# Performance work log

Measured on AMD Instinct MI355X. Metric: run time of the kernel, lower is better.

## Reference

```python
import math
import jax, jax.numpy as jnp
import numpy as np

D_MODEL = 1024
D_STATE = 32
DT_MIN = 0.001
DT_MAX = 0.1
SEQ_LEN = 4096


def setup_inputs() -> dict:
    key = jax.random.key(0)
    kB, kC, kdt = jax.random.split(key, 3)
    log_A_real = jnp.full((D_MODEL, D_STATE), math.log(0.5), dtype=jnp.float32)
    A_imag = jnp.broadcast_to(jnp.linspace(0.0, math.pi, D_STATE, dtype=jnp.float32)[None, :],
                              (D_MODEL, D_STATE)).copy()
    B = jax.random.normal(kB, (D_MODEL, D_STATE, 2), dtype=jnp.float32)
    C = jax.random.normal(kC, (D_MODEL, D_STATE, 2), dtype=jnp.float32)
    log_dt = (jax.random.uniform(kdt, (D_MODEL,), dtype=jnp.float32)
              * (math.log(DT_MAX) - math.log(DT_MIN)) + math.log(DT_MIN))
    return {"log_A_real": log_A_real, "A_imag": A_imag, "B": B, "C": C,
            "log_dt": log_dt, "L": SEQ_LEN}


def reference(log_A_real, A_imag, B, C, log_dt, L):
    # ZOH-discretized diagonal SSM kernel: K[d,l] = Re(sum_n C[d,n] B[d,n] A_bar[d,n]^l)
    dt = jax.nn.softplus(log_dt)                      # (d,)
    A_real = -jax.nn.softplus(log_A_real)             # (d,n) forced negative
    A = jax.lax.complex(A_real, A_imag)               # (d,n) complex64
    A_bar = jnp.exp(dt[:, None] * A)                  # (d,n)
    Bc = jax.lax.complex(B[..., 0], B[..., 1])        # (d,n)
    Cc = jax.lax.complex(C[..., 0], C[..., 1])        # (d,n)
    l = jnp.arange(L, dtype=jnp.float32)              # (L,)
    # A_bar^l via exp(l*log(A_bar)); log(A_bar)=dt*A exactly since |dt*A_imag|<pi
    A_pow = jnp.exp((dt[:, None] * A)[:, :, None] * l)  # (d,n,L) Vandermonde
    K = jnp.einsum('dn,dnl->dl', Cc * Bc, A_pow).real   # (d,L)
    return K
```

## Files before the change

kernel.cpp:

```cpp
#include <hip/hip_runtime.h>
#include <math.h>

#define N_STATE 32

typedef _Float16 f16;
typedef f16 f16x8 __attribute__((ext_vector_type(8)));
typedef float f32x4 __attribute__((ext_vector_type(4)));

__device__ __forceinline__ unsigned swz(int row, int byte_in_row) {
  return (unsigned)(((row << 7) + byte_in_row) ^ ((row & 7) << 4));
}

__device__ __forceinline__ unsigned oswz(unsigned word) {
  return word ^ (((word >> 6) & 7u) << 2);
}

__device__ __forceinline__ float softplus_hw(float x) {
  const float t = __builtin_amdgcn_exp2f(x * 1.4426950408889634f);
  return 0.6931471805599453f * __builtin_amdgcn_logf(1.0f + t);
}

__global__ __launch_bounds__(256) void s4d_mfma_kernel(
    const float* __restrict__ log_A_real,
    const float* __restrict__ A_imag,
    const float* __restrict__ Bp,
    const float* __restrict__ Cp,
    const float* __restrict__ log_dt,
    float* __restrict__ K,
    int L) {
  const int d = blockIdx.x;
  const int tid = threadIdx.x;

  __shared__ float s_wrl2e[N_STATE], s_wirev[N_STATE];
  __shared__ float s_gr[N_STATE], s_gi[N_STATE];
  __shared__ __align__(16) char s_tab[2][64 * 128];
  f16* s_U = (f16*)s_tab[0];
  f16* s_V = (f16*)s_tab[1];
  float* s_out = (float*)s_tab;

  if (tid < N_STATE) {
    const int n = tid;
    const int idx = d * N_STATE + n;
    const float dt = softplus_hw(log_dt[d]);
    const float wr = -dt * softplus_hw(log_A_real[idx]);
    const float wi = dt * A_imag[idx];
    s_wrl2e[n] = wr * 1.4426950408889634f;
    s_wirev[n] = wi * 0.15915494309189535f;
    const float br = Bp[2 * idx], bi = Bp[2 * idx + 1];
    const float cr = Cp[2 * idx], ci = Cp[2 * idx + 1];
    s_gr[n] = cr * br - ci * bi;
    s_gi[n] = cr * bi + ci * br;
  }
  __syncthreads();

  {
    const int uh = tid >> 7;
    const int idx = tid & 127;
    const int row = idx & 63;
    const int nh = idx >> 6;
    const float sf = uh ? (float)row : (float)(row * 64);
    char* base = (char*)(uh ? s_V : s_U);
#pragma unroll
    for (int j = 0; j < 16; j += 2) {
      union { unsigned u32[2]; unsigned long long u64; } pk2;
#pragma unroll
      for (int jj = 0; jj < 2; ++jj) {
        const int n = nh * 16 + j + jj;
        const float er = __builtin_amdgcn_exp2f(s_wrl2e[n] * sf);
        const float ph = __builtin_amdgcn_fractf(s_wirev[n] * sf);
        const float cs = __builtin_amdgcn_cosf(ph);
        const float sn = __builtin_amdgcn_sinf(ph);
        const float zr = er * cs, zi = er * sn;
        float u0, u1;
        if (uh == 0) {
          u0 = s_gr[n] * zr - s_gi[n] * zi;
          u1 = s_gr[n] * zi + s_gi[n] * zr;
        } else {
          u0 = zr;
          u1 = -zi;
        }
        union { f16 h[2]; unsigned u; } pk;
        pk.h[0] = (f16)u0;
        pk.h[1] = (f16)u1;
        pk2.u32[jj] = pk.u;
      }
      *(unsigned long long*)(base + swz(row, (nh * 16 + j) * 4)) = pk2.u64;
    }
  }
  __syncthreads();

  const int wid = tid >> 6;
  const int lane = tid & 63;
  const int r = lane & 15;
  const int g = lane >> 4;

  f16x8 afrag[2];
#pragma unroll
  for (int kt = 0; kt < 2; ++kt)
    afrag[kt] = *(const f16x8*)((const char*)s_V +
                                swz(16 * wid + r, kt * 64 + g * 16));

  f32x4 acc[4];
#pragma unroll
  for (int nt = 0; nt < 4; ++nt) acc[nt] = (f32x4){0.f, 0.f, 0.f, 0.f};

#pragma unroll
  for (int nt = 0; nt < 4; ++nt) {
#pragma unroll
    for (int kt = 0; kt < 2; ++kt) {
      const f16x8 bfrag = *(const f16x8*)((const char*)s_U +
                                          swz(16 * nt + r, kt * 64 + g * 16));
      acc[nt] = __builtin_amdgcn_mfma_f32_16x16x32_f16(afrag[kt], bfrag,
                                                       acc[nt], 0, 0, 0);
    }
  }

  __syncthreads();
#pragma unroll
  for (int nt = 0; nt < 4; ++nt) {
    const unsigned a = (unsigned)(16 * nt + r);
    const unsigned w = oswz(64u * a + (unsigned)(16 * wid + 4 * g));
    *(f32x4*)(s_out + w) = acc[nt];
  }
  __syncthreads();

  float* outd = K + (size_t)d * L;
#pragma unroll
  for (int i = 0; i < 4; ++i) {
    const unsigned f = (unsigned)(256 * i + tid);
    const f32x4 v = *(const f32x4*)(s_out + oswz(4u * f));
    __builtin_nontemporal_store(v, (f32x4*)(outd + 4u * f));
  }
}

extern "C" void kernel_launch(void* const* d_in, const int* in_sizes, int n_in,
                              void* d_out, int out_size, void* d_ws,
                              size_t ws_size, hipStream_t stream) {
  const float* log_A_real = (const float*)d_in[0];
  const float* A_imag = (const float*)d_in[1];
  const float* B = (const float*)d_in[2];
  const float* C = (const float*)d_in[3];
  const float* log_dt = (const float*)d_in[4];
  float* K = (float*)d_out;

  const int D = in_sizes[4];
  const int L = out_size / D;

  dim3 grid(D), block(256);
  hipLaunchKernelGGL(s4d_mfma_kernel, grid, block, 0, stream, log_A_real,
                     A_imag, B, C, log_dt, K, L);
}
```

Baseline: 10.76 us.

## Generate Vandermonde tables by complex recurrence per thread instead of per-entry transcendentals

Each thread now owns one state index and a block of 16 rows. It computes a base power and a step multiplier with transcendentals once, then fills its entries by repeated complex multiplication. This drops the per-entry exp/sin/cos and removes the shared-memory parameter staging and one barrier. It also packs values with cvt_pkrtz, which rounds toward zero. The cost is recurrence error accumulating over 16 steps, plus narrower 4-byte LDS stores in place of 8-byte ones.

New measurement: 10.39 us. 1.04x faster.

```diff
diff --git a/kernel.cpp b/kernel.cpp
--- a/kernel.cpp
+++ b/kernel.cpp
@@ -4,6 +4,7 @@
 #define N_STATE 32
 
 typedef _Float16 f16;
+typedef __fp16 fp16x2 __attribute__((ext_vector_type(2)));
 typedef f16 f16x8 __attribute__((ext_vector_type(8)));
 typedef float f32x4 __attribute__((ext_vector_type(4)));
 
@@ -31,60 +32,57 @@
   const int d = blockIdx.x;
   const int tid = threadIdx.x;
 
-  __shared__ float s_wrl2e[N_STATE], s_wirev[N_STATE];
-  __shared__ float s_gr[N_STATE], s_gi[N_STATE];
   __shared__ __align__(16) char s_tab[2][64 * 128];
   f16* s_U = (f16*)s_tab[0];
   f16* s_V = (f16*)s_tab[1];
   float* s_out = (float*)s_tab;
 
-  if (tid < N_STATE) {
-    const int n = tid;
+  {
+    const int uh = tid >> 7;
+    const int n = tid & 31;
+    const int rblk = (tid >> 5) & 3;
     const int idx = d * N_STATE + n;
+
     const float dt = softplus_hw(log_dt[d]);
     const float wr = -dt * softplus_hw(log_A_real[idx]);
     const float wi = dt * A_imag[idx];
-    s_wrl2e[n] = wr * 1.4426950408889634f;
-    s_wirev[n] = wi * 0.15915494309189535f;
-    const float br = Bp[2 * idx], bi = Bp[2 * idx + 1];
-    const float cr = Cp[2 * idx], ci = Cp[2 * idx + 1];
-    s_gr[n] = cr * br - ci * bi;
-    s_gi[n] = cr * bi + ci * br;
-  }
-  __syncthreads();
+    const float wrl2e = wr * 1.4426950408889634f;
+    const float wirev = wi * 0.15915494309189535f;
 
-  {
-    const int uh = tid >> 7;
-    const int idx = tid & 127;
-    const int row = idx & 63;
-    const int nh = idx >> 6;
-    const float sf = uh ? (float)row : (float)(row * 64);
-    char* base = (char*)(uh ? s_V : s_U);
+    const float sf0 = uh ? (float)(16 * rblk) : (float)(1024 * rblk);
+    const float sst = uh ? 1.0f : 64.0f;
+    const float eb = __builtin_amdgcn_exp2f(wrl2e * sf0);
+    const float phb = __builtin_amdgcn_fractf(wirev * sf0);
+    float pr = eb * __builtin_amdgcn_cosf(phb);
+    float pq = eb * __builtin_amdgcn_sinf(phb);
+    const float em = __builtin_amdgcn_exp2f(wrl2e * sst);
+    const float phm = __builtin_amdgcn_fractf(wirev * sst);
+    float mr = em * __builtin_amdgcn_cosf(phm);
+    float mi = em * __builtin_amdgcn_sinf(phm);
+
+    if (uh == 0) {
+      const float br = Bp[2 * idx], bi = Bp[2 * idx + 1];
+      const float cr = Cp[2 * idx], ci = Cp[2 * idx + 1];
+      const float gr = cr * br - ci * bi;
+      const float gi = cr * bi + ci * br;
+      const float tr = gr * pr - gi * pq;
+      pq = gr * pq + gi * pr;
+      pr = tr;
+    } else {
+      pq = -pq;
+      mi = -mi;
+    }
+
+    char* tab = s_tab[uh];
+    const int r0 = 16 * rblk;
 #pragma unroll
-    for (int j = 0; j < 16; j += 2) {
-      union { unsigned u32[2]; unsigned long long u64; } pk2;
-#pragma unroll
-      for (int jj = 0; jj < 2; ++jj) {
-        const int n = nh * 16 + j + jj;
-        const float er = __builtin_amdgcn_exp2f(s_wrl2e[n] * sf);
-        const float ph = __builtin_amdgcn_fractf(s_wirev[n] * sf);
-        const float cs = __builtin_amdgcn_cosf(ph);
-        const float sn = __builtin_amdgcn_sinf(ph);
-        const float zr = er * cs, zi = er * sn;
-        float u0, u1;
-        if (uh == 0) {
-          u0 = s_gr[n] * zr - s_gi[n] * zi;
-          u1 = s_gr[n] * zi + s_gi[n] * zr;
-        } else {
-          u0 = zr;
-          u1 = -zi;
-        }
-        union { f16 h[2]; unsigned u; } pk;
-        pk.h[0] = (f16)u0;
-        pk.h[1] = (f16)u1;
-        pk2.u32[jj] = pk.u;
-      }
-      *(unsigned long long*)(base + swz(row, (nh * 16 + j) * 4)) = pk2.u64;
+    for (int j = 0; j < 16; ++j) {
+      union { fp16x2 v; unsigned u; } pk;
+      pk.v = __builtin_amdgcn_cvt_pkrtz(pr, pq);
+      *(unsigned*)(tab + swz(r0 + j, 4 * n)) = pk.u;
+      const float nr = pr * mr - pq * mi;
+      pq = pr * mi + pq * mr;
+      pr = nr;
     }
   }
   __syncthreads();
```
